# Performance work log

Hardware: AMD Instinct MI355X
Metric: run time of the kernel (lower is better)

Reference implementation:

```python
import jax, jax.numpy as jnp
import numpy as np

S = 4096      # sequence length
E = 256       # embedding_dim
H = 256       # hidden_dim // 2 (per direction)
T = 16        # tagset size
V = 100000    # vocab size
START = 14
STOP = 15
NEG = -10000.0


def setup_inputs() -> dict:
    key = jax.random.key(0)
    ks = jax.random.split(key, 16)
    trans = jax.random.normal(ks[12], (T, T), jnp.float32)
    trans = trans.at[START, :].set(NEG).at[:, STOP].set(NEG)
    return {
        "sentence": jax.random.randint(ks[0], (S,), 0, V),
        "embed": jax.random.normal(ks[1], (V, E), jnp.float32),
        "W_ih_f": jax.random.normal(ks[2], (4 * H, E), jnp.float32) * 0.05,
        "W_hh_f": jax.random.normal(ks[3], (4 * H, H), jnp.float32) * 0.05,
        "b_ih_f": jax.random.normal(ks[4], (4 * H,), jnp.float32) * 0.05,
        "b_hh_f": jax.random.normal(ks[5], (4 * H,), jnp.float32) * 0.05,
        "W_ih_b": jax.random.normal(ks[6], (4 * H, E), jnp.float32) * 0.05,
        "W_hh_b": jax.random.normal(ks[7], (4 * H, H), jnp.float32) * 0.05,
        "b_ih_b": jax.random.normal(ks[8], (4 * H,), jnp.float32) * 0.05,
        "b_hh_b": jax.random.normal(ks[9], (4 * H,), jnp.float32) * 0.05,
        "W_out": jax.random.normal(ks[10], (T, 2 * H), jnp.float32) * 0.05,
        "b_out": jax.random.normal(ks[11], (T,), jnp.float32) * 0.05,
        "transitions": trans,
        "h0": jax.random.normal(ks[13], (2, H), jnp.float32),
        "c0": jax.random.normal(ks[14], (2, H), jnp.float32),
    }


def _lstm(x, h0, c0, W_ih, W_hh, b_ih, b_hh):
    """Single-direction LSTM over x:[S,E]; PyTorch gate order i,f,g,o."""
    b = b_ih + b_hh
    xg = x @ W_ih.T + b  # [S, 4H] precompute input contribution

    def step(carry, xt):
        h, c = carry
        g = xt + h @ W_hh.T
        i, f, gg, o = jnp.split(g, 4)
        i = jax.nn.sigmoid(i)
        f = jax.nn.sigmoid(f)
        gg = jnp.tanh(gg)
        o = jax.nn.sigmoid(o)
        c = f * c + i * gg
        h = o * jnp.tanh(c)
        return (h, c), h

    _, hs = jax.lax.scan(step, (h0, c0), xg)
    return hs  # [S, H]


def reference(sentence, embed, W_ih_f, W_hh_f, b_ih_f, b_hh_f,
              W_ih_b, W_hh_b, b_ih_b, b_hh_b, W_out, b_out,
              transitions, h0, c0):
    x = embed[sentence]  # [S, E]
    hf = _lstm(x, h0[0], c0[0], W_ih_f, W_hh_f, b_ih_f, b_hh_f)
    hb = _lstm(x[::-1], h0[1], c0[1], W_ih_b, W_hh_b, b_ih_b, b_hh_b)[::-1]
    feats = jnp.concatenate([hf, hb], axis=-1) @ W_out.T + b_out  # [S, T]

    # CRF forward algorithm (log partition). transitions[i, j] = score j -> i.
    alpha0 = jnp.full((T,), NEG, feats.dtype).at[START].set(0.0)

    def crf_step(alpha, emit):
        a = jax.nn.logsumexp(alpha[None, :] + transitions, axis=1) + emit
        return a, None

    alpha, _ = jax.lax.scan(crf_step, alpha0, feats)
    return jax.nn.logsumexp(alpha + transitions[STOP])
```

## Files before the change

### kernel.cpp

```cpp
#include <hip/hip_runtime.h>
#include <hip/hip_bf16.h>

#define S 4096
#define E 256
#define HH 256
#define TT 16
#define NEG_ -10000.0f
#define START_ 14
#define STOP_ 15
#define DSTRIDE_F (S * 256 + 256)

__device__ __forceinline__ float fast_exp(float x) {
    return __builtin_amdgcn_exp2f(x * 1.4426950408889634f);
}
__device__ __forceinline__ float fast_log(float x) {
    return 0.6931471805599453f * __builtin_amdgcn_logf(x);
}

__global__ __launch_bounds__(64) void quant4_kernel(
    const float* __restrict__ Wf, const float* __restrict__ Wb,
    const float* __restrict__ h0,
    int* __restrict__ wq4, float* __restrict__ wscale,
    int* __restrict__ hq0p)
{
    int blk = blockIdx.x, lane = threadIdx.x;
    const float* src;
    int* dst;
    float* scl = nullptr;
    bool fixed = false;
    if (blk < 2048) {
        int d = blk >> 10, r = blk & 1023;
        src = (d == 0 ? Wf : Wb) + (size_t)r * 256;
        dst = wq4 + ((size_t)(d * 1024 + r)) * 32;
        scl = wscale + (d * 1024 + r);
    } else {
        int d = blk - 2048;
        src = h0 + (size_t)d * 256;
        dst = hq0p + d * 32;
        fixed = true;
    }
    float4 a = make_float4(0.f, 0.f, 0.f, 0.f), b = a;
    if (lane < 32) {
        a = ((const float4*)src)[2 * lane];
        b = ((const float4*)src)[2 * lane + 1];
    }
    float f[8] = {a.x, a.y, a.z, a.w, b.x, b.y, b.z, b.w};
    float m = 0.f;
    #pragma unroll
    for (int k = 0; k < 8; ++k) m = fmaxf(m, fabsf(f[k]));
    #pragma unroll
    for (int off = 1; off < 64; off <<= 1) m = fmaxf(m, __shfl_xor(m, off, 64));
    m = fmaxf(m, 1e-20f);
    float inv = fixed ? 7.0f : (7.0f / m);
    if (lane < 32) {
        int dw = 0;
        #pragma unroll
        for (int k = 0; k < 8; ++k) {
            int q = __float2int_rn(f[k] * inv);
            q = max(-8, min(7, q));
            dw |= (q & 0xF) << (4 * k);
        }
        dst[lane] = dw;
    }
    if (!fixed && lane == 0) *scl = m / 7.0f;
}

__global__ __launch_bounds__(256) void transpose_kernel(
    const float* __restrict__ Wf, const float* __restrict__ Wb,
    float* __restrict__ WT)
{
    __shared__ float tile[32][33];
    const int dir = blockIdx.z;
    const float* W = dir ? Wb : Wf;
    const int r0 = blockIdx.x * 32, e0 = blockIdx.y * 32;
    const int tr = threadIdx.x & 31, tc = threadIdx.x >> 5;
    #pragma unroll
    for (int i = 0; i < 32; i += 8)
        tile[tc + i][tr] = W[(size_t)(r0 + tc + i) * 256 + e0 + tr];
    __syncthreads();
    float* out = WT + (size_t)dir * 256 * 1024;
    #pragma unroll
    for (int i = 0; i < 32; i += 8)
        out[(size_t)(e0 + tc + i) * 1024 + r0 + tr] = tile[tr][tc + i];
}

__global__ __launch_bounds__(256) void xg_kernel(
    const int* __restrict__ sent, const float* __restrict__ embed,
    const float* __restrict__ WT,
    const float* __restrict__ bihf, const float* __restrict__ bhhf,
    const float* __restrict__ bihb, const float* __restrict__ bhhb,
    float* __restrict__ xg)
{
    const int dir = blockIdx.y;
    const int t0 = blockIdx.x * 16;
    const int tid = threadIdx.x;
    const float* Wt = WT + (size_t)dir * 256 * 1024;
    __shared__ float xt[16][256];
    for (int tt = 0; tt < 16; ++tt) {
        int t = t0 + tt;
        int pos = dir ? (S - 1 - t) : t;
        int w = sent[pos];
        xt[tt][tid] = embed[(size_t)w * 256 + tid];
    }
    __syncthreads();
    float acc[4][16];
    #pragma unroll
    for (int rc = 0; rc < 4; ++rc)
        #pragma unroll
        for (int tt = 0; tt < 16; ++tt) acc[rc][tt] = 0.f;
    for (int e = 0; e < 256; ++e) {
        float xv[16];
        #pragma unroll
        for (int tt = 0; tt < 16; ++tt) xv[tt] = xt[tt][e];
        const float* wrow = Wt + (size_t)e * 1024;
        #pragma unroll
        for (int rc = 0; rc < 4; ++rc) {
            float w = wrow[rc * 256 + tid];
            #pragma unroll
            for (int tt = 0; tt < 16; ++tt) acc[rc][tt] += w * xv[tt];
        }
    }
    const float* bih = dir ? bihb : bihf;
    const float* bhh = dir ? bhhb : bhhf;
    float b0 = bih[0 * 256 + tid] + bhh[0 * 256 + tid];
    float b1 = bih[1 * 256 + tid] + bhh[1 * 256 + tid];
    float b2 = bih[2 * 256 + tid] + bhh[2 * 256 + tid];
    float b3 = bih[3 * 256 + tid] + bhh[3 * 256 + tid];
    #pragma unroll
    for (int tt = 0; tt < 16; ++tt) {
        float4 v;
        v.x = acc[0][tt] + b0;
        v.y = acc[1][tt] + b1;
        v.z = acc[2][tt] + b2;
        v.w = acc[3][tt] + b3;
        ((float4*)(xg + ((size_t)dir * S + (t0 + tt)) * 1024))[tid] = v;
    }
}

#define D8(a,w,h) "v_dot8_i32_i4 " a ", " w ", " h ", " a "\n\t"
#define CH(H0,H1,H2,H3, I0,I1,I2,I3, F0,F1,F2,F3, G0,G1,G2,G3, O0,O1,O2,O3) \
 D8("v192",I0,H0) D8("v193",F0,H0) D8("v194",G0,H0) D8("v195",O0,H0) \
 D8("v192",I1,H1) D8("v193",F1,H1) D8("v194",G1,H1) D8("v195",O1,H1) \
 D8("v192",I2,H2) D8("v193",F2,H2) D8("v194",G2,H2) D8("v195",O2,H2) \
 D8("v192",I3,H3) D8("v193",F3,H3) D8("v194",G3,H3) D8("v195",O3,H3)

#define LSTM_BODY(XI, XF, XG, XO, NQUAD) \
  "ds_read_b128 v[160:163], v206\n\t" \
  "ds_read_b128 v[164:167], v206 offset:16\n\t" \
  "ds_read_b128 v[168:171], v206 offset:32\n\t" \
  "ds_read_b128 v[172:175], v206 offset:48\n\t" \
  "ds_read_b128 v[176:179], v206 offset:64\n\t" \
  "ds_read_b128 v[180:183], v206 offset:80\n\t" \
  "ds_read_b128 v[184:187], v206 offset:96\n\t" \
  "ds_read_b128 v[188:191], v206 offset:112\n\t" \
  "v_xor_b32 v206, 0x80, v206\n\t" \
  "global_store_dword v205, v218, %[shs]\n\t" \
  "v_add_u32 v205, 0x400, v205\n\t" \
  "global_load_dwordx4 " NQUAD ", v204, %[sxg]\n\t" \
  "v_add_u32 v204, 0x1000, v204\n\t" \
  "s_waitcnt lgkmcnt(7)\n\t" \
  CH("v160","v161","v162","v163", "v32","v33","v34","v35", "v64","v65","v66","v67", "v96","v97","v98","v99", "v128","v129","v130","v131") \
  "s_waitcnt lgkmcnt(6)\n\t" \
  CH("v164","v165","v166","v167", "v36","v37","v38","v39", "v68","v69","v70","v71", "v100","v101","v102","v103", "v132","v133","v134","v135") \
  "s_waitcnt lgkmcnt(5)\n\t" \
  CH("v168","v169","v170","v171", "v40","v41","v42","v43", "v72","v73","v74","v75", "v104","v105","v106","v107", "v136","v137","v138","v139") \
  "s_waitcnt lgkmcnt(4)\n\t" \
  CH("v172","v173","v174","v175", "v44","v45","v46","v47", "v76","v77","v78","v79", "v108","v109","v110","v111", "v140","v141","v142","v143") \
  "s_waitcnt lgkmcnt(3)\n\t" \
  CH("v176","v177","v178","v179", "v48","v49","v50","v51", "v80","v81","v82","v83", "v112","v113","v114","v115", "v144","v145","v146","v147") \
  "s_waitcnt lgkmcnt(2)\n\t" \
  CH("v180","v181","v182","v183", "v52","v53","v54","v55", "v84","v85","v86","v87", "v116","v117","v118","v119", "v148","v149","v150","v151") \
  "s_waitcnt lgkmcnt(1)\n\t" \
  CH("v184","v185","v186","v187", "v56","v57","v58","v59", "v88","v89","v90","v91", "v120","v121","v122","v123", "v152","v153","v154","v155") \
  "s_waitcnt lgkmcnt(0)\n\t" \
  CH("v188","v189","v190","v191", "v60","v61","v62","v63", "v92","v93","v94","v95", "v124","v125","v126","v127", "v156","v157","v158","v159") \
  "v_cvt_f32_i32 v208, v192\n\t" \
  "v_cvt_f32_i32 v209, v193\n\t" \
  "v_cvt_f32_i32 v210, v194\n\t" \
  "v_cvt_f32_i32 v211, v195\n\t" \
  "s_waitcnt vmcnt(2)\n\t" \
  "v_fma_f32 v212, %[sci], v208, " XI "\n\t" \
  "v_fma_f32 v213, %[scf], v209, " XF "\n\t" \
  "v_fma_f32 v214, %[scg], v210, " XG "\n\t" \
  "v_fma_f32 v215, %[sco], v211, " XO "\n\t" \
  "v_mul_f32 v208, %[nk], v212\n\t" \
  "v_mul_f32 v209, %[nk], v213\n\t" \
  "v_mul_f32 v211, %[nk], v215\n\t" \
  "v_med3_f32 v214, v214, %[ncl], %[pcl]\n\t" \
  "v_mul_f32 v210, %[k2], v214\n\t" \
  "v_exp_f32 v208, v208\n\t" \
  "v_exp_f32 v209, v209\n\t" \
  "v_exp_f32 v211, v211\n\t" \
  "v_exp_f32 v210, v210\n\t" \
  "s_nop 1\n\t" \
  "v_add_f32 v212, 1.0, v208\n\t" \
  "v_add_f32 v213, 1.0, v209\n\t" \
  "v_add_f32 v215, 1.0, v211\n\t" \
  "v_add_f32 v216, 1.0, v210\n\t" \
  "v_add_f32 v217, -1.0, v210\n\t" \
  "v_rcp_f32 v212, v212\n\t" \
  "v_rcp_f32 v213, v213\n\t" \
  "v_rcp_f32 v215, v215\n\t" \
  "v_rcp_f32 v216, v216\n\t" \
  "s_nop 1\n\t" \
  "v_mul_f32 v217, v217, v216\n\t" \
  "v_mul_f32 v219, %[c7], v215\n\t" \
  "v_mul_f32 v220, v213, v220\n\t" \
  "v_fmac_f32 v220, v212, v217\n\t" \
  "v_med3_f32 v208, v220, %[ncl], %[pcl]\n\t" \
  "v_mul_f32 v208, %[k2], v208\n\t" \
  "v_exp_f32 v208, v208\n\t" \
  "s_nop 1\n\t" \
  "v_add_f32 v209, -1.0, v208\n\t" \
  "v_add_f32 v210, 1.0, v208\n\t" \
  "v_rcp_f32 v210, v210\n\t" \
  "s_nop 1\n\t" \
  "v_mul_f32 v209, v209, v210\n\t" \
  "v_mul_f32 v217, v219, v209\n\t" \
  "v_add_f32 v208, 0x4b400000, v217\n\t" \
  "v_and_b32 v208, 15, v208\n\t" \
  "v_lshlrev_b32 v208, v225, v208\n\t" \
  "v_mul_f32 v218, %[i7], v217\n\t" \
  "s_nop 1\n\t" \
  "v_mov_b32_dpp v209, v208 quad_perm:[1,0,3,2] row_mask:0xf bank_mask:0xf\n\t" \
  "v_or_b32 v208, v208, v209\n\t" \
  "s_nop 1\n\t" \
  "v_mov_b32_dpp v209, v208 quad_perm:[2,3,0,1] row_mask:0xf bank_mask:0xf\n\t" \
  "v_or_b32 v208, v208, v209\n\t" \
  "ds_write_b16 v207, v208\n\t" \
  "v_xor_b32 v207, 0x80, v207\n\t" \
  "v_mov_b32 v192, 0\n\t" \
  "v_mov_b32 v193, 0\n\t" \
  "v_mov_b32 v194, 0\n\t" \
  "v_mov_b32 v195, 0\n\t" \
  "s_waitcnt lgkmcnt(0)\n\t" \
  "s_barrier\n\t"

__global__ __launch_bounds__(256, 1) void lstm_kernel(
    const float* __restrict__ xg, const int* __restrict__ wq4,
    const float* __restrict__ wscale, const int* __restrict__ hq0p,
    const float* __restrict__ c0, float* __restrict__ hs)
{
    const int d = blockIdx.x;
    const int t = threadIdx.x;

    __shared__ alignas(16) int hq4buf[512];

    const int*   wq_d = wq4 + (size_t)d * 32768;
    const float* xg_d = xg + (size_t)d * S * 1024;
    float*       hs_d = hs + (size_t)d * DSTRIDE_F;
    const float sci = wscale[d * 1024 + t]       * (1.0f / 7.0f);
    const float scf = wscale[d * 1024 + 256 + t] * (1.0f / 7.0f);
    const float scg = wscale[d * 1024 + 512 + t] * (1.0f / 7.0f);
    const float sco = wscale[d * 1024 + 768 + t] * (1.0f / 7.0f);
    const float c0v = c0[d * 256 + t];
    const int h0v = hq0p[d * 32 + (t & 31)];
    const unsigned h0a = (t < 32) ? (unsigned)t * 4u : (1536u + (unsigned)(t & 63) * 4u);
    const unsigned xai = (unsigned)t * 16u;
    const unsigned hsi = (unsigned)t * 4u;
    const unsigned wad = ((t & 3) == 0) ? (128u + (unsigned)(t >> 1))
                                        : (512u + (unsigned)((t & 255) << 2));
    const unsigned voW = (unsigned)t * 128u;
    const unsigned shf = (unsigned)(t & 3) * 4u;
    const float nk = -1.4426950408889634f;
    const float k2 = 2.8853900817779268f;
    const float c7 = 7.0f;
    const float i7 = 1.0f / 7.0f;
    const float ncl = -30.0f, pcl = 30.0f;
    const unsigned lds_keep = (unsigned)(size_t)&hq4buf[0];
    int cnt = S / 2;

    asm volatile(
        "v_mov_b32 v204, %[xai]\n\t"
        "v_mov_b32 v205, %[hsi]\n\t"
        "v_mov_b32 v206, 0\n\t"
        "v_mov_b32 v207, %[wad]\n\t"
        "v_mov_b32 v218, 0\n\t"
        "v_mov_b32 v220, %[c0v]\n\t"
        "v_mov_b32 v225, %[shf]\n\t"
        "v_mov_b32 v192, 0\n\t"
        "v_mov_b32 v193, 0\n\t"
        "v_mov_b32 v194, 0\n\t"
        "v_mov_b32 v195, 0\n\t"
        "ds_write_b32 %[h0a], %[h0v]\n\t"
        "v_mov_b32 v208, %[voW]\n\t"
        "global_load_dwordx4 v[32:35], v208, %[swq]\n\t"
        "global_load_dwordx4 v[36:39], v208, %[swq] offset:16\n\t"
        "global_load_dwordx4 v[40:43], v208, %[swq] offset:32\n\t"
        "global_load_dwordx4 v[44:47], v208, %[swq] offset:48\n\t"
        "global_load_dwordx4 v[48:51], v208, %[swq] offset:64\n\t"
        "global_load_dwordx4 v[52:55], v208, %[swq] offset:80\n\t"
        "global_load_dwordx4 v[56:59], v208, %[swq] offset:96\n\t"
        "global_load_dwordx4 v[60:63], v208, %[swq] offset:112\n\t"
        "v_add_u32 v208, 0x8000, v208\n\t"
        "global_load_dwordx4 v[64:67], v208, %[swq]\n\t"
        "global_load_dwordx4 v[68:71], v208, %[swq] offset:16\n\t"
        "global_load_dwordx4 v[72:75], v208, %[swq] offset:32\n\t"
        "global_load_dwordx4 v[76:79], v208, %[swq] offset:48\n\t"
        "global_load_dwordx4 v[80:83], v208, %[swq] offset:64\n\t"
        "global_load_dwordx4 v[84:87], v208, %[swq] offset:80\n\t"
        "global_load_dwordx4 v[88:91], v208, %[swq] offset:96\n\t"
        "global_load_dwordx4 v[92:95], v208, %[swq] offset:112\n\t"
        "v_add_u32 v208, 0x8000, v208\n\t"
        "global_load_dwordx4 v[96:99],   v208, %[swq]\n\t"
        "global_load_dwordx4 v[100:103], v208, %[swq] offset:16\n\t"
        "global_load_dwordx4 v[104:107], v208, %[swq] offset:32\n\t"
        "global_load_dwordx4 v[108:111], v208, %[swq] offset:48\n\t"
        "global_load_dwordx4 v[112:115], v208, %[swq] offset:64\n\t"
        "global_load_dwordx4 v[116:119], v208, %[swq] offset:80\n\t"
        "global_load_dwordx4 v[120:123], v208, %[swq] offset:96\n\t"
        "global_load_dwordx4 v[124:127], v208, %[swq] offset:112\n\t"
        "v_add_u32 v208, 0x8000, v208\n\t"
        "global_load_dwordx4 v[128:131], v208, %[swq]\n\t"
        "global_load_dwordx4 v[132:135], v208, %[swq] offset:16\n\t"
        "global_load_dwordx4 v[136:139], v208, %[swq] offset:32\n\t"
        "global_load_dwordx4 v[140:143], v208, %[swq] offset:48\n\t"
        "global_load_dwordx4 v[144:147], v208, %[swq] offset:64\n\t"
        "global_load_dwordx4 v[148:151], v208, %[swq] offset:80\n\t"
        "global_load_dwordx4 v[152:155], v208, %[swq] offset:96\n\t"
        "global_load_dwordx4 v[156:159], v208, %[swq] offset:112\n\t"
        "global_load_dwordx4 v[196:199], v204, %[sxg]\n\t"
        "v_add_u32 v204, 0x1000, v204\n\t"
        "s_waitcnt vmcnt(0) lgkmcnt(0)\n\t"
        "s_barrier\n\t"
        "Llstm%=:\n\t"
        LSTM_BODY("v196", "v197", "v198", "v199", "v[200:203]")
        LSTM_BODY("v200", "v201", "v202", "v203", "v[196:199]")
        "s_add_i32 %[cnt], %[cnt], -1\n\t"
        "s_cmp_lg_u32 %[cnt], 0\n\t"
        "s_cbranch_scc1 Llstm%=\n\t"
        "global_store_dword v205, v218, %[shs]\n\t"
        : [cnt] "+s"(cnt)
        : [sxg] "s"(xg_d), [shs] "s"(hs_d), [swq] "s"(wq_d),
          [xai] "v"(xai), [hsi] "v"(hsi), [wad] "v"(wad),
          [c0v] "v"(c0v), [h0a] "v"(h0a), [h0v] "v"(h0v),
          [sci] "v"(sci), [scf] "v"(scf), [scg] "v"(scg), [sco] "v"(sco),
          [nk] "v"(nk), [k2] "v"(k2), [c7] "v"(c7), [i7] "v"(i7),
          [ncl] "v"(ncl), [pcl] "v"(pcl),
          [voW] "v"(voW), [shf] "v"(shf), [keep] "v"(lds_keep)
        : "memory", "scc",
          "v32","v33","v34","v35","v36","v37","v38","v39",
          "v40","v41","v42","v43","v44","v45","v46","v47",
          "v48","v49","v50","v51","v52","v53","v54","v55",
          "v56","v57","v58","v59","v60","v61","v62","v63",
          "v64","v65","v66","v67","v68","v69","v70","v71",
          "v72","v73","v74","v75","v76","v77","v78","v79",
          "v80","v81","v82","v83","v84","v85","v86","v87",
          "v88","v89","v90","v91","v92","v93","v94","v95",
          "v96","v97","v98","v99","v100","v101","v102","v103",
          "v104","v105","v106","v107","v108","v109","v110","v111",
          "v112","v113","v114","v115","v116","v117","v118","v119",
          "v120","v121","v122","v123","v124","v125","v126","v127",
          "v128","v129","v130","v131","v132","v133","v134","v135",
          "v136","v137","v138","v139","v140","v141","v142","v143",
          "v144","v145","v146","v147","v148","v149","v150","v151",
          "v152","v153","v154","v155","v156","v157","v158","v159",
          "v160","v161","v162","v163","v164","v165","v166","v167",
          "v168","v169","v170","v171","v172","v173","v174","v175",
          "v176","v177","v178","v179","v180","v181","v182","v183",
          "v184","v185","v186","v187","v188","v189","v190","v191",
          "v192","v193","v194","v195","v196","v197","v198","v199",
          "v200","v201","v202","v203","v204","v205","v206","v207",
          "v208","v209","v210","v211","v212","v213","v214","v215",
          "v216","v217","v218","v219","v220","v221","v222","v223",
          "v224","v225");
}

__global__ __launch_bounds__(256) void feats_kernel(
    const float* __restrict__ hsf, const float* __restrict__ hsb,
    const float* __restrict__ Wout,
    const float* __restrict__ bout, float* __restrict__ feats)
{
    __shared__ float Wl[16][513];
    int tid = threadIdx.x;
    for (int i = tid; i < 16 * 512; i += 256) Wl[i >> 9][i & 511] = Wout[i];
    __syncthreads();
    int tt = tid >> 4, tag = tid & 15;
    int tcur = blockIdx.x * 16 + tt;
    const float* hf = hsf + (size_t)tcur * 256;
    const float* hb = hsb + (size_t)(S - 1 - tcur) * 256;
    float acc = bout[tag];
    for (int k = 0; k < 256; ++k) acc += Wl[tag][k] * hf[k];
    for (int k = 0; k < 256; ++k) acc += Wl[tag][256 + k] * hb[k];
    feats[(size_t)tcur * 16 + tag] = acc;
}

__global__ __launch_bounds__(256) void crf_chunk_kernel(
    const float* __restrict__ feats, const float* __restrict__ trans,
    float* __restrict__ P)
{
    int chunk = blockIdx.x;
    int tid = threadIdx.x;
    int i = tid >> 4, jj = tid & 15;
    __shared__ float Mt[2][16][17];
    float tr[16];
    #pragma unroll
    for (int k = 0; k < 16; ++k) tr[k] = trans[i * 16 + k];
    int t0 = chunk * 64;
    float emit = feats[(size_t)t0 * 16 + i];
    Mt[0][jj][i] = tr[jj] + emit;
    __syncthreads();
    int cur = 0;
    float em_next = feats[(size_t)(t0 + 1) * 16 + i];
    for (int s = 1; s < 64; ++s) {
        float em = em_next;
        if (s + 1 < 64) em_next = feats[(size_t)(t0 + s + 1) * 16 + i];
        float v[16];
        #pragma unroll
        for (int k = 0; k < 16; ++k) v[k] = tr[k] + Mt[cur][jj][k];
        float m = v[0];
        #pragma unroll
        for (int k = 1; k < 16; ++k) m = fmaxf(m, v[k]);
        float ssum = 0.f;
        #pragma unroll
        for (int k = 0; k < 16; ++k) ssum += fast_exp(v[k] - m);
        float nv = em + m + fast_log(ssum);
        Mt[cur ^ 1][jj][i] = nv;
        cur ^= 1;
        __syncthreads();
    }
    P[((size_t)chunk * 16 + i) * 16 + jj] = Mt[cur][jj][i];
}

__global__ __launch_bounds__(256) void crf_fold_kernel(
    const float* __restrict__ P, const float* __restrict__ trans,
    float* __restrict__ out)
{
    int tid = threadIdx.x;
    int i = tid >> 4, jj = tid & 15;
    __shared__ float alpha[16];
    if (tid < 16) alpha[tid] = (tid == START_) ? 0.0f : NEG_;
    __syncthreads();
    for (int cc = 0; cc < 64; ++cc) {
        float pv = P[((size_t)cc * 16 + i) * 16 + jj];
        float v = pv + alpha[jj];
        float m = v;
        #pragma unroll
        for (int off = 1; off < 16; off <<= 1) m = fmaxf(m, __shfl_xor(m, off, 64));
        float e = fast_exp(v - m);
        #pragma unroll
        for (int off = 1; off < 16; off <<= 1) e += __shfl_xor(e, off, 64);
        float nv = m + fast_log(e);
        __syncthreads();
        if (jj == 0) alpha[i] = nv;
        __syncthreads();
    }
    if (tid < 16) {
        float v = alpha[tid] + trans[STOP_ * 16 + tid];
        float m = v;
        #pragma unroll
        for (int off = 1; off < 16; off <<= 1) m = fmaxf(m, __shfl_xor(m, off, 64));
        float e = fast_exp(v - m);
        #pragma unroll
        for (int off = 1; off < 16; off <<= 1) e += __shfl_xor(e, off, 64);
        if (tid == 0) out[0] = m + fast_log(e);
    }
}

extern "C" void kernel_launch(void* const* d_in, const int* in_sizes, int n_in,
                              void* d_out, int out_size, void* d_ws, size_t ws_size,
                              hipStream_t stream) {
    const int*   sent  = (const int*)d_in[0];
    const float* embed = (const float*)d_in[1];
    const float* Wihf  = (const float*)d_in[2];
    const float* Whhf  = (const float*)d_in[3];
    const float* bihf  = (const float*)d_in[4];
    const float* bhhf  = (const float*)d_in[5];
    const float* Wihb  = (const float*)d_in[6];
    const float* Whhb  = (const float*)d_in[7];
    const float* bihb  = (const float*)d_in[8];
    const float* bhhb  = (const float*)d_in[9];
    const float* Wout  = (const float*)d_in[10];
    const float* bout  = (const float*)d_in[11];
    const float* trans = (const float*)d_in[12];
    const float* h0    = (const float*)d_in[13];
    const float* c0    = (const float*)d_in[14];
    float* out = (float*)d_out;

    char* ws = (char*)d_ws;
    constexpr size_t OFF_XG     = 0;
    constexpr size_t OFF_WQ     = OFF_XG + (size_t)2 * S * 1024 * 4;
    constexpr size_t OFF_WSCALE = OFF_WQ + (size_t)2 * 1024 * 32 * 4;
    constexpr size_t OFF_HQ0    = OFF_WSCALE + 2 * 1024 * 4;
    constexpr size_t OFF_WT     = OFF_HQ0 + 256;
    constexpr size_t OFF_HS     = OFF_WT + (size_t)2 * 256 * 1024 * 4;
    constexpr size_t OFF_FEATS  = OFF_HS + (size_t)2 * DSTRIDE_F * 4;
    constexpr size_t OFF_P      = OFF_FEATS + (size_t)S * 16 * 4;

    float* xg     = (float*)(ws + OFF_XG);
    int*   wq4    = (int*)(ws + OFF_WQ);
    float* wscale = (float*)(ws + OFF_WSCALE);
    int*   hq0p   = (int*)(ws + OFF_HQ0);
    float* WT     = (float*)(ws + OFF_WT);
    float* hs     = (float*)(ws + OFF_HS);
    float* feats  = (float*)(ws + OFF_FEATS);
    float* P      = (float*)(ws + OFF_P);

    quant4_kernel<<<dim3(2050), dim3(64), 0, stream>>>(Whhf, Whhb, h0, wq4, wscale, hq0p);
    transpose_kernel<<<dim3(32, 8, 2), dim3(256), 0, stream>>>(Wihf, Wihb, WT);
    xg_kernel<<<dim3(256, 2), dim3(256), 0, stream>>>(sent, embed, WT, bihf, bhhf,
                                                      bihb, bhhb, xg);
    lstm_kernel<<<dim3(2), dim3(256), 0, stream>>>(xg, wq4, wscale, hq0p, c0, hs);
    feats_kernel<<<dim3(256), dim3(256), 0, stream>>>(hs + 256, hs + DSTRIDE_F + 256,
                                                      Wout, bout, feats);
    crf_chunk_kernel<<<dim3(64), dim3(256), 0, stream>>>(feats, trans, P);
    crf_fold_kernel<<<dim3(1), dim3(256), 0, stream>>>(P, trans, out);
}
```

Before: 2.154 ms.

## Split LSTM recurrent dot products across two thread halves with LDS reduction

The recurrent LSTM kernel now launches 512 threads per direction instead of 256. Each half of the block handles half of the hidden-dimension K range with int4 dot products, then the halves exchange partial sums through shared memory behind an extra barrier before the gate nonlinearities. This halves the per-thread serial dot-product chain and register footprint on the latency-bound sequential scan. In exchange it adds an LDS write/read round trip and a second barrier per timestep, and both halves redundantly compute the gate math.

After: 2.803 ms. 30.1% more time.

```diff
diff --git a/kernel.cpp b/kernel.cpp
--- a/kernel.cpp
+++ b/kernel.cpp
@@ -138,129 +138,131 @@
 }
 
 #define D8(a,w,h) "v_dot8_i32_i4 " a ", " w ", " h ", " a "\n\t"
-#define CH(H0,H1,H2,H3, I0,I1,I2,I3, F0,F1,F2,F3, G0,G1,G2,G3, O0,O1,O2,O3) \
- D8("v192",I0,H0) D8("v193",F0,H0) D8("v194",G0,H0) D8("v195",O0,H0) \
- D8("v192",I1,H1) D8("v193",F1,H1) D8("v194",G1,H1) D8("v195",O1,H1) \
- D8("v192",I2,H2) D8("v193",F2,H2) D8("v194",G2,H2) D8("v195",O2,H2) \
- D8("v192",I3,H3) D8("v193",F3,H3) D8("v194",G3,H3) D8("v195",O3,H3)
+#define CHK(H0,H1,H2,H3, I0,I1,I2,I3, F0,F1,F2,F3, G0,G1,G2,G3, O0,O1,O2,O3) \
+ D8("v112",I0,H0) D8("v113",F0,H0) D8("v114",G0,H0) D8("v115",O0,H0) \
+ D8("v112",I1,H1) D8("v113",F1,H1) D8("v114",G1,H1) D8("v115",O1,H1) \
+ D8("v112",I2,H2) D8("v113",F2,H2) D8("v114",G2,H2) D8("v115",O2,H2) \
+ D8("v112",I3,H3) D8("v113",F3,H3) D8("v114",G3,H3) D8("v115",O3,H3)
 
 #define LSTM_BODY(XI, XF, XG, XO, NQUAD) \
-  "ds_read_b128 v[160:163], v206\n\t" \
-  "ds_read_b128 v[164:167], v206 offset:16\n\t" \
-  "ds_read_b128 v[168:171], v206 offset:32\n\t" \
-  "ds_read_b128 v[172:175], v206 offset:48\n\t" \
-  "ds_read_b128 v[176:179], v206 offset:64\n\t" \
-  "ds_read_b128 v[180:183], v206 offset:80\n\t" \
-  "ds_read_b128 v[184:187], v206 offset:96\n\t" \
-  "ds_read_b128 v[188:191], v206 offset:112\n\t" \
-  "v_xor_b32 v206, 0x80, v206\n\t" \
-  "global_store_dword v205, v218, %[shs]\n\t" \
-  "v_add_u32 v205, 0x400, v205\n\t" \
-  "global_load_dwordx4 " NQUAD ", v204, %[sxg]\n\t" \
-  "v_add_u32 v204, 0x1000, v204\n\t" \
-  "s_waitcnt lgkmcnt(7)\n\t" \
-  CH("v160","v161","v162","v163", "v32","v33","v34","v35", "v64","v65","v66","v67", "v96","v97","v98","v99", "v128","v129","v130","v131") \
-  "s_waitcnt lgkmcnt(6)\n\t" \
-  CH("v164","v165","v166","v167", "v36","v37","v38","v39", "v68","v69","v70","v71", "v100","v101","v102","v103", "v132","v133","v134","v135") \
-  "s_waitcnt lgkmcnt(5)\n\t" \
-  CH("v168","v169","v170","v171", "v40","v41","v42","v43", "v72","v73","v74","v75", "v104","v105","v106","v107", "v136","v137","v138","v139") \
-  "s_waitcnt lgkmcnt(4)\n\t" \
-  CH("v172","v173","v174","v175", "v44","v45","v46","v47", "v76","v77","v78","v79", "v108","v109","v110","v111", "v140","v141","v142","v143") \
+  "ds_read_b128 v[96:99],   v126\n\t" \
+  "ds_read_b128 v[100:103], v126 offset:16\n\t" \
+  "ds_read_b128 v[104:107], v126 offset:32\n\t" \
+  "ds_read_b128 v[108:111], v126 offset:48\n\t" \
+  "v_xor_b32 v126, 0x80, v126\n\t" \
+  "global_store_dword v125, v147, %[shs]\n\t" \
+  "v_add_u32 v125, 0x400, v125\n\t" \
+  "global_load_dwordx4 " NQUAD ", v124, %[sxg]\n\t" \
+  "v_add_u32 v124, 0x1000, v124\n\t" \
   "s_waitcnt lgkmcnt(3)\n\t" \
-  CH("v176","v177","v178","v179", "v48","v49","v50","v51", "v80","v81","v82","v83", "v112","v113","v114","v115", "v144","v145","v146","v147") \
+  CHK("v96","v97","v98","v99", "v32","v33","v34","v35", "v48","v49","v50","v51", "v64","v65","v66","v67", "v80","v81","v82","v83") \
   "s_waitcnt lgkmcnt(2)\n\t" \
-  CH("v180","v181","v182","v183", "v52","v53","v54","v55", "v84","v85","v86","v87", "v116","v117","v118","v119", "v148","v149","v150","v151") \
+  CHK("v100","v101","v102","v103", "v36","v37","v38","v39", "v52","v53","v54","v55", "v68","v69","v70","v71", "v84","v85","v86","v87") \
   "s_waitcnt lgkmcnt(1)\n\t" \
-  CH("v184","v185","v186","v187", "v56","v57","v58","v59", "v88","v89","v90","v91", "v120","v121","v122","v123", "v152","v153","v154","v155") \
+  CHK("v104","v105","v106","v107", "v40","v41","v42","v43", "v56","v57","v58","v59", "v72","v73","v74","v75", "v88","v89","v90","v91") \
   "s_waitcnt lgkmcnt(0)\n\t" \
-  CH("v188","v189","v190","v191", "v60","v61","v62","v63", "v92","v93","v94","v95", "v124","v125","v126","v127", "v156","v157","v158","v159") \
-  "v_cvt_f32_i32 v208, v192\n\t" \
-  "v_cvt_f32_i32 v209, v193\n\t" \
-  "v_cvt_f32_i32 v210, v194\n\t" \
-  "v_cvt_f32_i32 v211, v195\n\t" \
+  CHK("v108","v109","v110","v111", "v44","v45","v46","v47", "v60","v61","v62","v63", "v76","v77","v78","v79", "v92","v93","v94","v95") \
+  "ds_write_b128 v128, v[112:115]\n\t" \
+  "s_waitcnt lgkmcnt(0)\n\t" \
+  "s_barrier\n\t" \
+  "ds_read_b128 v[130:133], v129\n\t" \
+  "s_waitcnt lgkmcnt(0)\n\t" \
+  "v_add_u32 v112, v112, v130\n\t" \
+  "v_add_u32 v113, v113, v131\n\t" \
+  "v_add_u32 v114, v114, v132\n\t" \
+  "v_add_u32 v115, v115, v133\n\t" \
+  "v_cvt_f32_i32 v134, v112\n\t" \
+  "v_cvt_f32_i32 v135, v113\n\t" \
+  "v_cvt_f32_i32 v136, v114\n\t" \
+  "v_cvt_f32_i32 v137, v115\n\t" \
   "s_waitcnt vmcnt(2)\n\t" \
-  "v_fma_f32 v212, %[sci], v208, " XI "\n\t" \
-  "v_fma_f32 v213, %[scf], v209, " XF "\n\t" \
-  "v_fma_f32 v214, %[scg], v210, " XG "\n\t" \
-  "v_fma_f32 v215, %[sco], v211, " XO "\n\t" \
-  "v_mul_f32 v208, %[nk], v212\n\t" \
-  "v_mul_f32 v209, %[nk], v213\n\t" \
-  "v_mul_f32 v211, %[nk], v215\n\t" \
-  "v_med3_f32 v214, v214, %[ncl], %[pcl]\n\t" \
-  "v_mul_f32 v210, %[k2], v214\n\t" \
-  "v_exp_f32 v208, v208\n\t" \
-  "v_exp_f32 v209, v209\n\t" \
-  "v_exp_f32 v211, v211\n\t" \
-  "v_exp_f32 v210, v210\n\t" \
-  "s_nop 1\n\t" \
-  "v_add_f32 v212, 1.0, v208\n\t" \
-  "v_add_f32 v213, 1.0, v209\n\t" \
-  "v_add_f32 v215, 1.0, v211\n\t" \
-  "v_add_f32 v216, 1.0, v210\n\t" \
-  "v_add_f32 v217, -1.0, v210\n\t" \
-  "v_rcp_f32 v212, v212\n\t" \
-  "v_rcp_f32 v213, v213\n\t" \
-  "v_rcp_f32 v215, v215\n\t" \
-  "v_rcp_f32 v216, v216\n\t" \
-  "s_nop 1\n\t" \
-  "v_mul_f32 v217, v217, v216\n\t" \
-  "v_mul_f32 v219, %[c7], v215\n\t" \
-  "v_mul_f32 v220, v213, v220\n\t" \
-  "v_fmac_f32 v220, v212, v217\n\t" \
-  "v_med3_f32 v208, v220, %[ncl], %[pcl]\n\t" \
-  "v_mul_f32 v208, %[k2], v208\n\t" \
-  "v_exp_f32 v208, v208\n\t" \
-  "s_nop 1\n\t" \
-  "v_add_f32 v209, -1.0, v208\n\t" \
-  "v_add_f32 v210, 1.0, v208\n\t" \
-  "v_rcp_f32 v210, v210\n\t" \
-  "s_nop 1\n\t" \
-  "v_mul_f32 v209, v209, v210\n\t" \
-  "v_mul_f32 v217, v219, v209\n\t" \
-  "v_add_f32 v208, 0x4b400000, v217\n\t" \
-  "v_and_b32 v208, 15, v208\n\t" \
-  "v_lshlrev_b32 v208, v225, v208\n\t" \
-  "v_mul_f32 v218, %[i7], v217\n\t" \
-  "s_nop 1\n\t" \
-  "v_mov_b32_dpp v209, v208 quad_perm:[1,0,3,2] row_mask:0xf bank_mask:0xf\n\t" \
-  "v_or_b32 v208, v208, v209\n\t" \
-  "s_nop 1\n\t" \
-  "v_mov_b32_dpp v209, v208 quad_perm:[2,3,0,1] row_mask:0xf bank_mask:0xf\n\t" \
-  "v_or_b32 v208, v208, v209\n\t" \
-  "ds_write_b16 v207, v208\n\t" \
-  "v_xor_b32 v207, 0x80, v207\n\t" \
-  "v_mov_b32 v192, 0\n\t" \
-  "v_mov_b32 v193, 0\n\t" \
-  "v_mov_b32 v194, 0\n\t" \
-  "v_mov_b32 v195, 0\n\t" \
+  "v_fma_f32 v138, %[sci], v134, " XI "\n\t" \
+  "v_fma_f32 v139, %[scf], v135, " XF "\n\t" \
+  "v_fma_f32 v140, %[scg], v136, " XG "\n\t" \
+  "v_fma_f32 v141, %[sco], v137, " XO "\n\t" \
+  "v_mul_f32 v134, %[nk], v138\n\t" \
+  "v_mul_f32 v135, %[nk], v139\n\t" \
+  "v_mul_f32 v137, %[nk], v141\n\t" \
+  "v_med3_f32 v140, v140, %[ncl], %[pcl]\n\t" \
+  "v_mul_f32 v136, %[k2], v140\n\t" \
+  "v_exp_f32 v134, v134\n\t" \
+  "v_exp_f32 v135, v135\n\t" \
+  "v_exp_f32 v137, v137\n\t" \
+  "v_exp_f32 v136, v136\n\t" \
+  "s_nop 1\n\t" \
+  "v_add_f32 v138, 1.0, v134\n\t" \
+  "v_add_f32 v139, 1.0, v135\n\t" \
+  "v_add_f32 v141, 1.0, v137\n\t" \
+  "v_add_f32 v142, 1.0, v136\n\t" \
+  "v_add_f32 v143, -1.0, v136\n\t" \
+  "v_rcp_f32 v138, v138\n\t" \
+  "v_rcp_f32 v139, v139\n\t" \
+  "v_rcp_f32 v141, v141\n\t" \
+  "v_rcp_f32 v142, v142\n\t" \
+  "s_nop 1\n\t" \
+  "v_mul_f32 v143, v143, v142\n\t" \
+  "v_mul_f32 v144, %[c7], v141\n\t" \
+  "v_mul_f32 v146, v139, v146\n\t" \
+  "v_fmac_f32 v146, v138, v143\n\t" \
+  "v_med3_f32 v134, v146, %[ncl], %[pcl]\n\t" \
+  "v_mul_f32 v134, %[k2], v134\n\t" \
+  "v_exp_f32 v134, v134\n\t" \
+  "s_nop 1\n\t" \
+  "v_add_f32 v135, -1.0, v134\n\t" \
+  "v_add_f32 v136, 1.0, v134\n\t" \
+  "v_rcp_f32 v136, v136\n\t" \
+  "s_nop 1\n\t" \
+  "v_mul_f32 v135, v135, v136\n\t" \
+  "v_mul_f32 v143, v144, v135\n\t" \
+  "v_add_f32 v134, 0x4b400000, v143\n\t" \
+  "v_and_b32 v134, 15, v134\n\t" \
+  "v_lshlrev_b32 v134, v148, v134\n\t" \
+  "v_mul_f32 v147, %[i7], v143\n\t" \
+  "s_nop 1\n\t" \
+  "v_mov_b32_dpp v135, v134 quad_perm:[1,0,3,2] row_mask:0xf bank_mask:0xf\n\t" \
+  "v_or_b32 v134, v134, v135\n\t" \
+  "s_nop 1\n\t" \
+  "v_mov_b32_dpp v135, v134 quad_perm:[2,3,0,1] row_mask:0xf bank_mask:0xf\n\t" \
+  "v_or_b32 v134, v134, v135\n\t" \
+  "ds_write_b16 v127, v134\n\t" \
+  "v_xor_b32 v127, 0x80, v127\n\t" \
+  "v_mov_b32 v112, 0\n\t" \
+  "v_mov_b32 v113, 0\n\t" \
+  "v_mov_b32 v114, 0\n\t" \
+  "v_mov_b32 v115, 0\n\t" \
   "s_waitcnt lgkmcnt(0)\n\t" \
   "s_barrier\n\t"
 
-__global__ __launch_bounds__(256, 1) void lstm_kernel(
+__global__ __launch_bounds__(512, 2) void lstm_kernel(
     const float* __restrict__ xg, const int* __restrict__ wq4,
     const float* __restrict__ wscale, const int* __restrict__ hq0p,
     const float* __restrict__ c0, float* __restrict__ hs)
 {
     const int d = blockIdx.x;
     const int t = threadIdx.x;
-
-    __shared__ alignas(16) int hq4buf[512];
+    const int m = t & 255;
+    const int kh = t >> 8;
+
+    __shared__ alignas(16) int hq4buf[2432];
 
     const int*   wq_d = wq4 + (size_t)d * 32768;
     const float* xg_d = xg + (size_t)d * S * 1024;
     float*       hs_d = hs + (size_t)d * DSTRIDE_F;
-    const float sci = wscale[d * 1024 + t]       * (1.0f / 7.0f);
-    const float scf = wscale[d * 1024 + 256 + t] * (1.0f / 7.0f);
-    const float scg = wscale[d * 1024 + 512 + t] * (1.0f / 7.0f);
-    const float sco = wscale[d * 1024 + 768 + t] * (1.0f / 7.0f);
-    const float c0v = c0[d * 256 + t];
+    const float sci = wscale[d * 1024 + m]       * (1.0f / 7.0f);
+    const float scf = wscale[d * 1024 + 256 + m] * (1.0f / 7.0f);
+    const float scg = wscale[d * 1024 + 512 + m] * (1.0f / 7.0f);
+    const float sco = wscale[d * 1024 + 768 + m] * (1.0f / 7.0f);
+    const float c0v = c0[d * 256 + m];
     const int h0v = hq0p[d * 32 + (t & 31)];
-    const unsigned h0a = (t < 32) ? (unsigned)t * 4u : (1536u + (unsigned)(t & 63) * 4u);
-    const unsigned xai = (unsigned)t * 16u;
-    const unsigned hsi = (unsigned)t * 4u;
-    const unsigned wad = ((t & 3) == 0) ? (128u + (unsigned)(t >> 1))
-                                        : (512u + (unsigned)((t & 255) << 2));
-    const unsigned voW = (unsigned)t * 128u;
+    const unsigned dmp = 9216u + (unsigned)(t & 127) * 4u;
+    const unsigned h0a = (t < 32) ? (unsigned)t * 4u : dmp;
+    const unsigned xai = (unsigned)m * 16u;
+    const unsigned hsi = (unsigned)m * 4u;
+    const unsigned hra = (unsigned)kh * 64u;
+    const unsigned hwa = (kh == 0 && (t & 3) == 0) ? (128u + (unsigned)(m >> 1)) : dmp;
+    const unsigned pwa = 1024u + (unsigned)kh * 4096u + (unsigned)m * 16u;
+    const unsigned pra = 1024u + (unsigned)(kh ^ 1) * 4096u + (unsigned)m * 16u;
+    const unsigned voW = (unsigned)m * 128u + (unsigned)kh * 64u;
     const unsigned shf = (unsigned)(t & 3) * 4u;
     const float nk = -1.4426950408889634f;
     const float k2 = 2.8853900817779268f;
@@ -271,68 +273,55 @@
     int cnt = S / 2;
 
     asm volatile(
-        "v_mov_b32 v204, %[xai]\n\t"
-        "v_mov_b32 v205, %[hsi]\n\t"
-        "v_mov_b32 v206, 0\n\t"
-        "v_mov_b32 v207, %[wad]\n\t"
-        "v_mov_b32 v218, 0\n\t"
-        "v_mov_b32 v220, %[c0v]\n\t"
-        "v_mov_b32 v225, %[shf]\n\t"
-        "v_mov_b32 v192, 0\n\t"
-        "v_mov_b32 v193, 0\n\t"
-        "v_mov_b32 v194, 0\n\t"
-        "v_mov_b32 v195, 0\n\t"
+        "v_mov_b32 v124, %[xai]\n\t"
+        "v_mov_b32 v125, %[hsi]\n\t"
+        "v_mov_b32 v126, %[hra]\n\t"
+        "v_mov_b32 v127, %[hwa]\n\t"
+        "v_mov_b32 v128, %[pwa]\n\t"
+        "v_mov_b32 v129, %[pra]\n\t"
+        "v_mov_b32 v146, %[c0v]\n\t"
+        "v_mov_b32 v147, 0\n\t"
+        "v_mov_b32 v148, %[shf]\n\t"
+        "v_mov_b32 v112, 0\n\t"
+        "v_mov_b32 v113, 0\n\t"
+        "v_mov_b32 v114, 0\n\t"
+        "v_mov_b32 v115, 0\n\t"
         "ds_write_b32 %[h0a], %[h0v]\n\t"
-        "v_mov_b32 v208, %[voW]\n\t"
-        "global_load_dwordx4 v[32:35], v208, %[swq]\n\t"
-        "global_load_dwordx4 v[36:39], v208, %[swq] offset:16\n\t"
-        "global_load_dwordx4 v[40:43], v208, %[swq] offset:32\n\t"
-        "global_load_dwordx4 v[44:47], v208, %[swq] offset:48\n\t"
-        "global_load_dwordx4 v[48:51], v208, %[swq] offset:64\n\t"
-        "global_load_dwordx4 v[52:55], v208, %[swq] offset:80\n\t"
-        "global_load_dwordx4 v[56:59], v208, %[swq] offset:96\n\t"
-        "global_load_dwordx4 v[60:63], v208, %[swq] offset:112\n\t"
-        "v_add_u32 v208, 0x8000, v208\n\t"
-        "global_load_dwordx4 v[64:67], v208, %[swq]\n\t"
-        "global_load_dwordx4 v[68:71], v208, %[swq] offset:16\n\t"
-        "global_load_dwordx4 v[72:75], v208, %[swq] offset:32\n\t"
-        "global_load_dwordx4 v[76:79], v208, %[swq] offset:48\n\t"
-        "global_load_dwordx4 v[80:83], v208, %[swq] offset:64\n\t"
-        "global_load_dwordx4 v[84:87], v208, %[swq] offset:80\n\t"
-        "global_load_dwordx4 v[88:91], v208, %[swq] offset:96\n\t"
-        "global_load_dwordx4 v[92:95], v208, %[swq] offset:112\n\t"
-        "v_add_u32 v208, 0x8000, v208\n\t"
-        "global_load_dwordx4 v[96:99],   v208, %[swq]\n\t"
-        "global_load_dwordx4 v[100:103], v208, %[swq] offset:16\n\t"
-        "global_load_dwordx4 v[104:107], v208, %[swq] offset:32\n\t"
-        "global_load_dwordx4 v[108:111], v208, %[swq] offset:48\n\t"
-        "global_load_dwordx4 v[112:115], v208, %[swq] offset:64\n\t"
-        "global_load_dwordx4 v[116:119], v208, %[swq] offset:80\n\t"
-        "global_load_dwordx4 v[120:123], v208, %[swq] offset:96\n\t"
-        "global_load_dwordx4 v[124:127], v208, %[swq] offset:112\n\t"
-        "v_add_u32 v208, 0x8000, v208\n\t"
-        "global_load_dwordx4 v[128:131], v208, %[swq]\n\t"
-        "global_load_dwordx4 v[132:135], v208, %[swq] offset:16\n\t"
-        "global_load_dwordx4 v[136:139], v208, %[swq] offset:32\n\t"
-        "global_load_dwordx4 v[140:143], v208, %[swq] offset:48\n\t"
-        "global_load_dwordx4 v[144:147], v208, %[swq] offset:64\n\t"
-        "global_load_dwordx4 v[148:151], v208, %[swq] offset:80\n\t"
-        "global_load_dwordx4 v[152:155], v208, %[swq] offset:96\n\t"
-        "global_load_dwordx4 v[156:159], v208, %[swq] offset:112\n\t"
-        "global_load_dwordx4 v[196:199], v204, %[sxg]\n\t"
-        "v_add_u32 v204, 0x1000, v204\n\t"
+        "v_mov_b32 v134, %[voW]\n\t"
+        "global_load_dwordx4 v[32:35], v134, %[swq]\n\t"
+        "global_load_dwordx4 v[36:39], v134, %[swq] offset:16\n\t"
+        "global_load_dwordx4 v[40:43], v134, %[swq] offset:32\n\t"
+        "global_load_dwordx4 v[44:47], v134, %[swq] offset:48\n\t"
+        "v_add_u32 v134, 0x8000, v134\n\t"
+        "global_load_dwordx4 v[48:51], v134, %[swq]\n\t"
+        "global_load_dwordx4 v[52:55], v134, %[swq] offset:16\n\t"
+        "global_load_dwordx4 v[56:59], v134, %[swq] offset:32\n\t"
+        "global_load_dwordx4 v[60:63], v134, %[swq] offset:48\n\t"
+        "v_add_u32 v134, 0x8000, v134\n\t"
+        "global_load_dwordx4 v[64:67], v134, %[swq]\n\t"
+        "global_load_dwordx4 v[68:71], v134, %[swq] offset:16\n\t"
+        "global_load_dwordx4 v[72:75], v134, %[swq] offset:32\n\t"
+        "global_load_dwordx4 v[76:79], v134, %[swq] offset:48\n\t"
+        "v_add_u32 v134, 0x8000, v134\n\t"
+        "global_load_dwordx4 v[80:83], v134, %[swq]\n\t"
+        "global_load_dwordx4 v[84:87], v134, %[swq] offset:16\n\t"
+        "global_load_dwordx4 v[88:91], v134, %[swq] offset:32\n\t"
+        "global_load_dwordx4 v[92:95], v134, %[swq] offset:48\n\t"
+        "global_load_dwordx4 v[116:119], v124, %[sxg]\n\t"
+        "v_add_u32 v124, 0x1000, v124\n\t"
         "s_waitcnt vmcnt(0) lgkmcnt(0)\n\t"
         "s_barrier\n\t"
         "Llstm%=:\n\t"
-        LSTM_BODY("v196", "v197", "v198", "v199", "v[200:203]")
-        LSTM_BODY("v200", "v201", "v202", "v203", "v[196:199]")
+        LSTM_BODY("v116", "v117", "v118", "v119", "v[120:123]")
+        LSTM_BODY("v120", "v121", "v122", "v123", "v[116:119]")
         "s_add_i32 %[cnt], %[cnt], -1\n\t"
         "s_cmp_lg_u32 %[cnt], 0\n\t"
         "s_cbranch_scc1 Llstm%=\n\t"
-        "global_store_dword v205, v218, %[shs]\n\t"
+        "global_store_dword v125, v147, %[shs]\n\t"
         : [cnt] "+s"(cnt)
         : [sxg] "s"(xg_d), [shs] "s"(hs_d), [swq] "s"(wq_d),
-          [xai] "v"(xai), [hsi] "v"(hsi), [wad] "v"(wad),
+          [xai] "v"(xai), [hsi] "v"(hsi), [hra] "v"(hra), [hwa] "v"(hwa),
+          [pwa] "v"(pwa), [pra] "v"(pra),
           [c0v] "v"(c0v), [h0a] "v"(h0a), [h0v] "v"(h0v),
           [sci] "v"(sci), [scf] "v"(scf), [scg] "v"(scg), [sco] "v"(sco),
           [nk] "v"(nk), [k2] "v"(k2), [c7] "v"(c7), [i7] "v"(i7),
@@ -353,17 +342,7 @@
           "v120","v121","v122","v123","v124","v125","v126","v127",
           "v128","v129","v130","v131","v132","v133","v134","v135",
           "v136","v137","v138","v139","v140","v141","v142","v143",
-          "v144","v145","v146","v147","v148","v149","v150","v151",
-          "v152","v153","v154","v155","v156","v157","v158","v159",
-          "v160","v161","v162","v163","v164","v165","v166","v167",
-          "v168","v169","v170","v171","v172","v173","v174","v175",
-          "v176","v177","v178","v179","v180","v181","v182","v183",
-          "v184","v185","v186","v187","v188","v189","v190","v191",
-          "v192","v193","v194","v195","v196","v197","v198","v199",
-          "v200","v201","v202","v203","v204","v205","v206","v207",
-          "v208","v209","v210","v211","v212","v213","v214","v215",
-          "v216","v217","v218","v219","v220","v221","v222","v223",
-          "v224","v225");
+          "v144","v145","v146","v147","v148");
 }
 
 __global__ __launch_bounds__(256) void feats_kernel(
@@ -500,7 +479,7 @@
     transpose_kernel<<<dim3(32, 8, 2), dim3(256), 0, stream>>>(Wihf, Wihb, WT);
     xg_kernel<<<dim3(256, 2), dim3(256), 0, stream>>>(sent, embed, WT, bihf, bhhf,
                                                       bihb, bhhb, xg);
-    lstm_kernel<<<dim3(2), dim3(256), 0, stream>>>(xg, wq4, wscale, hq0p, c0, hs);
+    lstm_kernel<<<dim3(2), dim3(512), 0, stream>>>(xg, wq4, wscale, hq0p, c0, hs);
     feats_kernel<<<dim3(256), dim3(256), 0, stream>>>(hs + 256, hs + DSTRIDE_F + 256,
                                                       Wout, bout, feats);
     crf_chunk_kernel<<<dim3(64), dim3(256), 0, stream>>>(feats, trans, P);
```
